# Optimization experiments

Measured on AMD Instinct MI355X. Metric: run time of the kernel, lower is better.

## Reference

```python
import jax, jax.numpy as jnp
import numpy as np

NUM_CLASSES = 20
NUM_ANCHORS = 3
BBOX_ATTRS = 5 + NUM_CLASSES
IMG_H = IMG_W = 416
IN_H = IN_W = 52
CONF_THRES = 0.5
NMS_THRES = 0.4
TOP_K = 2048


def setup_inputs() -> dict:
    key = jax.random.key(0)
    k1, _ = jax.random.split(key)
    inp = jax.random.normal(k1, (16, NUM_ANCHORS * BBOX_ATTRS, IN_H, IN_W), dtype=jnp.float32)
    anchors = jnp.array([[116.0, 90.0], [156.0, 198.0], [373.0, 326.0]], dtype=jnp.float32)
    return {"input": inp, "anchors": anchors}


def decode(inp, anchors):
    """YOLOv3 head decode (YOLOv3Loss.forward with targets=None).
    inp: [B, A*(5+C), H, W] -> output: [B, A*H*W, 5+C] with (cx, cy, w, h, conf, cls...)."""
    bs = inp.shape[0]
    stride_h = IMG_H / IN_H
    stride_w = IMG_W / IN_W
    scaled_anchors = anchors / jnp.array([stride_w, stride_h], dtype=inp.dtype)  # [A, 2]
    # [B, A, H, W, 5+C]
    pred = inp.reshape(bs, NUM_ANCHORS, BBOX_ATTRS, IN_H, IN_W).transpose(0, 1, 3, 4, 2)
    x = jax.nn.sigmoid(pred[..., 0])
    y = jax.nn.sigmoid(pred[..., 1])
    w = pred[..., 2]
    h = pred[..., 3]
    conf = jax.nn.sigmoid(pred[..., 4])
    pred_cls = jax.nn.sigmoid(pred[..., 5:])
    grid_x = jnp.arange(IN_W, dtype=inp.dtype)[None, None, None, :]
    grid_y = jnp.arange(IN_H, dtype=inp.dtype)[None, None, :, None]
    anchor_w = scaled_anchors[:, 0][None, :, None, None]
    anchor_h = scaled_anchors[:, 1][None, :, None, None]
    bx = (x + grid_x) * stride_w
    by = (y + grid_y) * stride_h
    bw = jnp.exp(w) * anchor_w * stride_w
    bh = jnp.exp(h) * anchor_h * stride_h
    boxes = jnp.stack([bx, by, bw, bh], axis=-1).reshape(bs, -1, 4)
    output = jnp.concatenate(
        [boxes, conf.reshape(bs, -1, 1), pred_cls.reshape(bs, -1, NUM_CLASSES)], axis=-1
    )
    return output


def _nms_one(corners, conf, cls_pred):
    """Greedy class-aware NMS over TOP_K conf-sorted candidates.
    corners: [K,4] x1y1x2y2, conf: [K] desc-sorted, cls_pred: [K] int32.
    Returns keep mask [K] bool."""
    x1, y1, x2, y2 = corners[:, 0], corners[:, 1], corners[:, 2], corners[:, 3]
    area = (x2 - x1 + 1.0) * (y2 - y1 + 1.0)
    ix1 = jnp.maximum(x1[:, None], x1[None, :])
    iy1 = jnp.maximum(y1[:, None], y1[None, :])
    ix2 = jnp.minimum(x2[:, None], x2[None, :])
    iy2 = jnp.minimum(y2[:, None], y2[None, :])
    inter = jnp.clip(ix2 - ix1 + 1.0, 0.0) * jnp.clip(iy2 - iy1 + 1.0, 0.0)
    iou = inter / (area[:, None] + area[None, :] - inter + 1e-16)
    # suppress j if kept i (earlier, higher conf, same class) overlaps >= thres
    cond = (iou >= NMS_THRES) & (cls_pred[:, None] == cls_pred[None, :])
    valid = conf >= CONF_THRES
    K = conf.shape[0]
    idx = jnp.arange(K)

    def body(i, carry):
        keep, supp = carry
        ki = valid[i] & (~supp[i])
        keep = keep.at[i].set(ki)
        supp = supp | (cond[i] & (idx > i) & ki)
        return keep, supp

    keep, _ = jax.lax.fori_loop(0, K, body, (jnp.zeros(K, bool), jnp.zeros(K, bool)))
    return keep


def reference(input, anchors):
    output = decode(input, anchors)  # [B, N, 5+C]
    conf = output[..., 4]
    # top-K candidates by objectness (desc order == conf sort in original NMS)
    top_conf, top_idx = jax.lax.top_k(conf, TOP_K)  # [B, K]
    boxes = output[..., :4]
    cx, cy, w, h = boxes[..., 0], boxes[..., 1], boxes[..., 2], boxes[..., 3]
    corners = jnp.stack([cx - w / 2, cy - h / 2, cx + w / 2, cy + h / 2], axis=-1)
    corners_s = jnp.take_along_axis(corners, top_idx[..., None], axis=1)  # [B, K, 4]
    cls_pred = jnp.argmax(output[..., 5:], axis=-1).astype(jnp.int32)  # [B, N]
    cls_s = jnp.take_along_axis(cls_pred, top_idx, axis=1)  # [B, K]
    keep = jax.vmap(_nms_one)(corners_s, top_conf, cls_s)  # [B, K] bool
    return output, top_idx, keep
```

## Files before the change

kernel.cpp:

```cpp
#include <hip/hip_runtime.h>

#pragma clang fp contract(off)

#define B 16
#define A 3
#define HGT 52
#define WID 52
#define HW 2704
#define NCAND 8112
#define CATTR 25
#define TOPK 2048
#define NWORD 64
#define CH 256
#define NCHUNK (TOPK / CH)
#define GPC (CH / 32)
#define CHP 260
#define EPT 8

typedef unsigned int uint32;
typedef unsigned long long u64;

__global__ __launch_bounds__(256) void decode_kernel(const float* __restrict__ inp,
                                                     const float* __restrict__ anchors,
                                                     float* __restrict__ out,
                                                     float* __restrict__ cws) {
    __shared__ float sm[256 * CATTR];
    int tid = threadIdx.x;
    int t = blockIdx.x * 256 + tid;
    int b  = t / NCAND;
    int n  = t - b * NCAND;
    int a  = n / HW;
    int hw = n - a * HW;
    int gy = hw / WID;
    int gx = hw - gy * WID;
    const float* ip = inp + ((size_t)(b * (A * CATTR) + a * CATTR)) * HW + hw;
    float* sp = sm + tid * CATTR;

    float p0 = ip[0 * HW], p1 = ip[1 * HW], p2 = ip[2 * HW], p3 = ip[3 * HW], p4 = ip[4 * HW];
    float sx = 1.0f / (1.0f + expf(-p0));
    float sy = 1.0f / (1.0f + expf(-p1));
    float bx = (sx + (float)gx) * 8.0f;
    float by = (sy + (float)gy) * 8.0f;
    float bw = expf(p2) * anchors[a * 2 + 0];
    float bh = expf(p3) * anchors[a * 2 + 1];
    float cf = 1.0f / (1.0f + expf(-p4));
    sp[0] = bx; sp[1] = by; sp[2] = bw; sp[3] = bh; sp[4] = cf;
    cws[t] = cf;
#pragma unroll
    for (int c = 0; c < 20; ++c) {
        float v = ip[(5 + c) * HW];
        sp[5 + c] = 1.0f / (1.0f + expf(-v));
    }
    __syncthreads();
    const float4* sm4 = (const float4*)sm;
    float4* o4 = (float4*)(out + (size_t)blockIdx.x * 256 * CATTR);
#pragma unroll
    for (int k = 0; k < 6; ++k) o4[k * 256 + tid] = sm4[k * 256 + tid];
    if (tid < 64) o4[1536 + tid] = sm4[1536 + tid];
}

__device__ __forceinline__ void cexd(u64& a, u64& b, bool up) {
    if ((a > b) == up) { u64 tmp = a; a = b; b = tmp; }
}

__device__ __forceinline__ u64 sel(u64 k, u64 o, bool kmin) {
    return kmin ? (k < o ? k : o) : (k > o ? k : o);
}

__device__ __forceinline__ void bitonic_merge_2048(u64 key[EPT], u64* mb, int t) {
    for (unsigned j = 1024; j >= 8; j >>= 1) {
        unsigned m = j >> 3;
        bool kmin = ((t & m) == 0);
        if (m >= 64) {
            __syncthreads();
#pragma unroll
            for (int e = 0; e < EPT; ++e) mb[e * 256 + t] = key[e];
            __syncthreads();
            int pt = t ^ (int)m;
#pragma unroll
            for (int e = 0; e < EPT; ++e) key[e] = sel(key[e], mb[e * 256 + pt], kmin);
        } else {
#pragma unroll
            for (int e = 0; e < EPT; ++e) {
                u64 o = __shfl_xor(key[e], (int)m);
                key[e] = sel(key[e], o, kmin);
            }
        }
    }
    cexd(key[0], key[4], true); cexd(key[1], key[5], true);
    cexd(key[2], key[6], true); cexd(key[3], key[7], true);
    cexd(key[0], key[2], true); cexd(key[1], key[3], true);
    cexd(key[4], key[6], true); cexd(key[5], key[7], true);
    cexd(key[0], key[1], true); cexd(key[2], key[3], true);
    cexd(key[4], key[5], true); cexd(key[6], key[7], true);
}

__global__ __launch_bounds__(256) void sort1_kernel(const float* __restrict__ conf,
                                                    u64* __restrict__ runs) {
    __shared__ u64 mb[2048];
    int blk = blockIdx.x;
    int b = blk >> 2, c = blk & 3;
    int t = threadIdx.x;
    int base = t * EPT;
    int gbase = c * 2048 + base;
    const float* cp = conf + b * NCAND;

    u64 key[EPT];
    if (gbase + EPT <= NCAND) {
        const float4* cp4 = (const float4*)(cp + gbase);
        float4 c0 = cp4[0], c1 = cp4[1];
        float cf[EPT] = {c0.x, c0.y, c0.z, c0.w, c1.x, c1.y, c1.z, c1.w};
#pragma unroll
        for (int e = 0; e < EPT; ++e) {
            unsigned bits = __float_as_uint(cf[e]) | 0x80000000u;
            key[e] = ((u64)(~bits) << 32) | (unsigned)(gbase + e);
        }
    } else {
#pragma unroll
        for (int e = 0; e < EPT; ++e) {
            int idx = gbase + e;
            if (idx < NCAND) {
                unsigned bits = __float_as_uint(cp[idx]) | 0x80000000u;
                key[e] = ((u64)(~bits) << 32) | (unsigned)idx;
            } else key[e] = ~0ull;
        }
    }

    cexd(key[0], key[1], true); cexd(key[2], key[3], false);
    cexd(key[4], key[5], true); cexd(key[6], key[7], false);

    cexd(key[0], key[2], true);  cexd(key[1], key[3], true);
    cexd(key[4], key[6], false); cexd(key[5], key[7], false);
    cexd(key[0], key[1], true);  cexd(key[2], key[3], true);
    cexd(key[4], key[5], false); cexd(key[6], key[7], false);

    bool up8 = ((t & 1) == 0);
    cexd(key[0], key[4], up8); cexd(key[1], key[5], up8);
    cexd(key[2], key[6], up8); cexd(key[3], key[7], up8);
    cexd(key[0], key[2], up8); cexd(key[1], key[3], up8);
    cexd(key[4], key[6], up8); cexd(key[5], key[7], up8);
    cexd(key[0], key[1], up8); cexd(key[2], key[3], up8);
    cexd(key[4], key[5], up8); cexd(key[6], key[7], up8);

    for (unsigned k = 16; k <= 2048; k <<= 1) {
        bool up = (((unsigned)base & k) == 0);
        for (unsigned j = k >> 1; j >= 8; j >>= 1) {
            unsigned m = j >> 3;
            bool kmin = (up == ((t & m) == 0));
            if (m >= 64) {
                __syncthreads();
#pragma unroll
                for (int e = 0; e < EPT; ++e) mb[e * 256 + t] = key[e];
                __syncthreads();
                int pt = t ^ (int)m;
#pragma unroll
                for (int e = 0; e < EPT; ++e) key[e] = sel(key[e], mb[e * 256 + pt], kmin);
            } else {
#pragma unroll
                for (int e = 0; e < EPT; ++e) {
                    u64 o = __shfl_xor(key[e], (int)m);
                    key[e] = sel(key[e], o, kmin);
                }
            }
        }
        cexd(key[0], key[4], up); cexd(key[1], key[5], up);
        cexd(key[2], key[6], up); cexd(key[3], key[7], up);
        cexd(key[0], key[2], up); cexd(key[1], key[3], up);
        cexd(key[4], key[6], up); cexd(key[5], key[7], up);
        cexd(key[0], key[1], up); cexd(key[2], key[3], up);
        cexd(key[4], key[5], up); cexd(key[6], key[7], up);
    }

    u64* R = runs + ((size_t)b * 4 + c) * 2048;
#pragma unroll
    for (int e = 0; e < EPT; ++e) R[base + e] = key[e];
}

__global__ __launch_bounds__(256) void sort23_kernel(const u64* __restrict__ runs,
                                                     const float* __restrict__ out,
                                                     float* __restrict__ topf,
                                                     float* __restrict__ gx1,
                                                     float* __restrict__ gy1,
                                                     float* __restrict__ gx2,
                                                     float* __restrict__ gy2,
                                                     float* __restrict__ gar,
                                                     uint32* __restrict__ gcv,
                                                     uint32* __restrict__ vwords) {
    __shared__ u64 mb[2048];
    __shared__ uint32 vb[256];
    int b = blockIdx.x;
    int t = threadIdx.x;
    int base = t * EPT;
    const u64* R0 = runs + (size_t)b * 4 * 2048;

    u64 ka[EPT], kb[EPT];
#pragma unroll
    for (int e = 0; e < EPT; ++e) {
        u64 a = R0[base + e];
        u64 o = R0[2048 + 2047 - (base + e)];
        ka[e] = a < o ? a : o;
    }
    bitonic_merge_2048(ka, mb, t);
#pragma unroll
    for (int e = 0; e < EPT; ++e) {
        u64 a = R0[2 * 2048 + base + e];
        u64 o = R0[3 * 2048 + 2047 - (base + e)];
        kb[e] = a < o ? a : o;
    }
    bitonic_merge_2048(kb, mb, t);
    __syncthreads();
#pragma unroll
    for (int e = 0; e < EPT; ++e) mb[base + e] = kb[e];
    __syncthreads();
#pragma unroll
    for (int e = 0; e < EPT; ++e) {
        u64 o = mb[2047 - (base + e)];
        ka[e] = ka[e] < o ? ka[e] : o;
    }
    bitonic_merge_2048(ka, mb, t);

    const float* ob = out + (size_t)b * NCAND * CATTR;
    uint32 vbits = 0;
#pragma unroll
    for (int e = 0; e < EPT; ++e) {
        uint32 idx = (uint32)(ka[e] & 0xFFFFFFFFu);
        int tg = b * TOPK + base + e;
        topf[tg] = (float)idx;
        const float* p = ob + (size_t)idx * CATTR;
        float cx = p[0], cy = p[1], w = p[2], h = p[3], cf = p[4];
        float hw_ = w * 0.5f, hh_ = h * 0.5f;
        float x1 = cx - hw_, y1 = cy - hh_, x2 = cx + hw_, y2 = cy + hh_;
        gx1[tg] = x1; gy1[tg] = y1; gx2[tg] = x2; gy2[tg] = y2;
        gar[tg] = ((x2 - x1) + 1.0f) * ((y2 - y1) + 1.0f);
        float best = p[5]; int bc = 0;
#pragma unroll
        for (int c = 1; c < 20; ++c) {
            float v = p[5 + c];
            if (v > best) { best = v; bc = c; }
        }
        gcv[tg] = (uint32)bc;
        vbits |= (cf >= 0.5f ? 1u : 0u) << e;
    }
    vb[t] = vbits;
    __syncthreads();
    if (t < 64) {
        uint32 w4 = vb[t * 4] | (vb[t * 4 + 1] << 8) | (vb[t * 4 + 2] << 16) | (vb[t * 4 + 3] << 24);
        vwords[b * 64 + t] = w4;
    }
}

#define KMID (13421772.5 / 33554432.0)
__global__ __launch_bounds__(1024) void build_kernel(const float* __restrict__ gx1,
                                                     const float* __restrict__ gy1,
                                                     const float* __restrict__ gx2,
                                                     const float* __restrict__ gy2,
                                                     const float* __restrict__ gar,
                                                     const uint32* __restrict__ gcv,
                                                     uint32* __restrict__ rowmask) {
    __shared__ float  x1s[TOPK], y1s[TOPK], x2s[TOPK], y2s[TOPK];
    __shared__ uint32 clss[TOPK];
    int bt   = blockIdx.y;
    int pr   = blockIdx.x;
    int tid  = threadIdx.x;
    int lane = tid & 63;
    int wv   = tid >> 6;
    int base = bt * TOPK;
    u64* rm64 = (u64*)(rowmask + (size_t)base * NWORD);

    for (int j = tid; j < TOPK; j += 1024) {
        int g = base + j;
        x1s[j] = gx1[g]; y1s[j] = gy1[g]; x2s[j] = gx2[g]; y2s[j] = gy2[g];
        clss[j] = gcv[g] & 0xffu;
    }
    __syncthreads();

    int r  = (wv >> 3) ? (31 - pr) : pr;
    int i0 = r * 64 + (wv & 7) * 8;

    float rx1[8], ry1[8], rx2[8], ry2[8], rar[8];
    uint32 rcl[8];
#pragma unroll
    for (int k = 0; k < 8; ++k) {
        rx1[k] = x1s[i0 + k]; ry1[k] = y1s[i0 + k];
        rx2[k] = x2s[i0 + k]; ry2[k] = y2s[i0 + k];
        rar[k] = ((rx2[k] - rx1[k]) + 1.0f) * ((ry2[k] - ry1[k]) + 1.0f);
        rcl[k] = clss[i0 + k];
    }

    int j0 = r * 64 + lane;
    float cx1 = x1s[j0], cy1 = y1s[j0], cx2 = x2s[j0], cy2 = y2s[j0];
    uint32 cc = clss[j0];

    for (int cg = r; cg < 32; ++cg) {
        float nx1 = 0.f, ny1 = 0.f, nx2 = 0.f, ny2 = 0.f; uint32 nc = 0;
        if (cg + 1 < 32) {
            int nj = (cg + 1) * 64 + lane;
            nx1 = x1s[nj]; ny1 = y1s[nj]; nx2 = x2s[nj]; ny2 = y2s[nj];
            nc = clss[nj];
        }
        float car = ((cx2 - cx1) + 1.0f) * ((cy2 - cy1) + 1.0f);
        u64 bal[8];
#pragma unroll
        for (int k = 0; k < 8; ++k) {
            float ix1 = fmaxf(rx1[k], cx1);
            float iy1 = fmaxf(ry1[k], cy1);
            float ix2 = fminf(rx2[k], cx2);
            float iy2 = fminf(ry2[k], cy2);
            float iw = fmaxf((ix2 - ix1) + 1.0f, 0.0f);
            float ih = fmaxf((iy2 - iy1) + 1.0f, 0.0f);
            float inter = iw * ih;
            float denom = ((rar[k] + car) - inter) + 1e-16f;
            bool cond = ((double)inter > KMID * (double)denom) && (cc == rcl[k]);
            bal[k] = __ballot(cond);
        }
        u64 v = bal[0];
#pragma unroll
        for (int k = 1; k < 8; ++k) if (lane == k) v = bal[k];
        if (lane < 8) rm64[(size_t)(i0 + lane) * 32 + cg] = v;
        cx1 = nx1; cy1 = ny1; cx2 = nx2; cy2 = ny2; cc = nc;
    }
}

__device__ __forceinline__ void copy_chunk(const uint32* __restrict__ rm,
                                           uint32* __restrict__ dst,
                                           int cc, int ctid) {
    const uint32* src = rm + (size_t)cc * CH * NWORD;
    int q4min = cc >> 1;
    for (int o = ctid; o < 1024; o += 960) {
        int q4 = o & 3, r = o >> 2;
        if (q4 < q4min) continue;
        const uint4* s4 = (const uint4*)(src + (size_t)r * NWORD + q4 * 16);
        uint4 v0 = s4[0], v1 = s4[1], v2 = s4[2], v3 = s4[3];
        int gi = cc * CH + r;
        int sg = gi >> 5;
        uint32 smsk = ~((2u << (gi & 31)) - 1u);
        uint32 wv[16] = {v0.x, v0.y, v0.z, v0.w, v1.x, v1.y, v1.z, v1.w,
                         v2.x, v2.y, v2.z, v2.w, v3.x, v3.y, v3.z, v3.w};
        int wbase = q4 * 16;
        uint32* dp = dst + r;
#pragma unroll
        for (int j = 0; j < 16; ++j) {
            uint32 x = wv[j];
            if (wbase + j == sg) x &= smsk;
            dp[(wbase + j) * CHP] = x;
        }
    }
}

__global__ __launch_bounds__(1024) void scan_kernel(const uint32* __restrict__ rowmask,
                                                    const uint32* __restrict__ vwords,
                                                    float* __restrict__ keepf) {
    __shared__ uint32 buf[2][64 * CHP];
    int bt  = blockIdx.x;
    int tid = threadIdx.x;
    int wv  = tid >> 6;
    int l   = tid & 63;
    const uint32* rm = rowmask + (size_t)bt * TOPK * NWORD;

    uint32 supp = 0, keepw = 0;
    if (wv == 0) supp = ~vwords[bt * 64 + l];

    if (wv > 0) copy_chunk(rm, buf[0], 0, tid - 64);
    __syncthreads();

    for (int c = 0; c < NCHUNK; ++c) {
        if (wv > 0) {
            if (c + 1 < NCHUNK) copy_chunk(rm, buf[(c + 1) & 1], c + 1, tid - 64);
        } else {
            const uint32* bp = buf[c & 1];
            uint4 sq[8];
            {
                int g0 = c * GPC;
                const uint4* sp = (const uint4*)(bp + g0 * CHP);
#pragma unroll
                for (int q = 0; q < 8; ++q) sq[q] = sp[q];
            }
            for (int gl = 0; gl < GPC; ++gl) {
                int g = c * GPC + gl;
                uint4 rwq[8];
                const uint4* rp = (const uint4*)(bp + l * CHP + gl * 32);
#pragma unroll
                for (int q = 0; q < 8; ++q) rwq[q] = rp[q];
                uint32 cur = __builtin_amdgcn_readlane(supp, g);
#pragma unroll
                for (int q = 0; q < 8; ++q) {
                    uint32 s0 = sq[q].x, s1 = sq[q].y, s2 = sq[q].z, s3 = sq[q].w;
                    int k = q * 4;
                    cur |= s0 & ((((cur >> (k + 0)) & 1u)) - 1u);
                    cur |= s1 & ((((cur >> (k + 1)) & 1u)) - 1u);
                    cur |= s2 & ((((cur >> (k + 2)) & 1u)) - 1u);
                    cur |= s3 & ((((cur >> (k + 3)) & 1u)) - 1u);
                }
                uint32 keep = ~cur;
                if (l == g) keepw = keep;
                if (gl + 1 < GPC) {
                    const uint4* sp = (const uint4*)(bp + (g + 1) * CHP + (gl + 1) * 32);
#pragma unroll
                    for (int q = 0; q < 8; ++q) sq[q] = sp[q];
                }
                uint32 upd = 0;
#pragma unroll
                for (int q = 0; q < 8; ++q) {
                    int k = q * 4;
                    upd |= rwq[q].x & (uint32)(((int)(keep << (31 - (k + 0)))) >> 31);
                    upd |= rwq[q].y & (uint32)(((int)(keep << (31 - (k + 1)))) >> 31);
                    upd |= rwq[q].z & (uint32)(((int)(keep << (31 - (k + 2)))) >> 31);
                    upd |= rwq[q].w & (uint32)(((int)(keep << (31 - (k + 3)))) >> 31);
                }
                supp |= upd;
            }
        }
        __syncthreads();
    }

    if (wv == 0) {
#pragma unroll
        for (int k = 0; k < 32; ++k)
            keepf[bt * TOPK + l * 32 + k] = (float)((keepw >> k) & 1u);
    }
}

extern "C" void kernel_launch(void* const* d_in, const int* in_sizes, int n_in,
                              void* d_out, int out_size, void* d_ws, size_t ws_size,
                              hipStream_t stream) {
    const float* inp     = (const float*)d_in[0];
    const float* anchors = (const float*)d_in[1];
    float* out   = (float*)d_out;
    float* topf  = out  + (size_t)B * NCAND * CATTR;
    float* keepf = topf + (size_t)B * TOPK;

    float*  cws = (float*)d_ws;
    float*  gx1 = cws + B * NCAND;
    float*  gy1 = gx1 + B * TOPK;
    float*  gx2 = gy1 + B * TOPK;
    float*  gy2 = gx2 + B * TOPK;
    float*  gar = gy2 + B * TOPK;
    uint32* gcv = (uint32*)(gar + B * TOPK);
    uint32* rowmask = gcv + B * TOPK;
    uint32* vwords  = rowmask + (size_t)B * TOPK * NWORD;
    u64* runs = (u64*)rowmask;

    decode_kernel<<<(B * NCAND) / 256, 256, 0, stream>>>(inp, anchors, out, cws);
    sort1_kernel<<<B * 4, 256, 0, stream>>>(cws, runs);
    sort23_kernel<<<B, 256, 0, stream>>>(runs, out, topf, gx1, gy1, gx2, gy2, gar, gcv, vwords);
    build_kernel<<<dim3(16, B), 1024, 0, stream>>>(gx1, gy1, gx2, gy2, gar, gcv, rowmask);
    scan_kernel<<<B, 1024, 0, stream>>>(rowmask, vwords, keepf);
}
```

Baseline: 186.5 us.

## Store suppression mask transposed and stream chunks via global_load_lds

The build kernel now writes the IoU suppression bitmask in a word-major (transposed) layout and applies the self/lower-triangle mask at write time. In return, the scan kernel's producer waves copy each chunk straight from global memory into LDS with the direct global_load_lds instruction, replacing the register-staged transpose and masking loop. This is meant to cut VGPR traffic and LDS write instructions in the copy path that overlaps the serial scan. The cost is narrower 32-bit scattered stores in the build kernel, and correctness depends on the LDS offset semantics of the direct-load builtin.

```diff
diff --git a/kernel.cpp b/kernel.cpp
--- a/kernel.cpp
+++ b/kernel.cpp
@@ -265,7 +265,7 @@
     int lane = tid & 63;
     int wv   = tid >> 6;
     int base = bt * TOPK;
-    u64* rm64 = (u64*)(rowmask + (size_t)base * NWORD);
+    uint32* rmT = rowmask + (size_t)base * NWORD;
 
     for (int j = tid; j < TOPK; j += 1024) {
         int g = base + j;
@@ -315,35 +315,25 @@
         }
         u64 v = bal[0];
 #pragma unroll
-        for (int k = 1; k < 8; ++k) if (lane == k) v = bal[k];
-        if (lane < 8) rm64[(size_t)(i0 + lane) * 32 + cg] = v;
+        for (int k = 1; k < 8; ++k) if ((lane & 7) == k) v = bal[k];
+        uint32 w32 = (lane & 8) ? (uint32)(v >> 32) : (uint32)v;
+        int gi = i0 + (lane & 7);
+        int wd = 2 * cg + ((lane >> 3) & 1);
+        if (wd == (gi >> 5)) w32 &= ~((2u << (gi & 31)) - 1u);
+        if (lane < 16) rmT[(size_t)wd * TOPK + gi] = w32;
         cx1 = nx1; cy1 = ny1; cx2 = nx2; cy2 = ny2; cc = nc;
     }
 }
 
-__device__ __forceinline__ void copy_chunk(const uint32* __restrict__ rm,
-                                           uint32* __restrict__ dst,
-                                           int cc, int ctid) {
-    const uint32* src = rm + (size_t)cc * CH * NWORD;
-    int q4min = cc >> 1;
-    for (int o = ctid; o < 1024; o += 960) {
-        int q4 = o & 3, r = o >> 2;
-        if (q4 < q4min) continue;
-        const uint4* s4 = (const uint4*)(src + (size_t)r * NWORD + q4 * 16);
-        uint4 v0 = s4[0], v1 = s4[1], v2 = s4[2], v3 = s4[3];
-        int gi = cc * CH + r;
-        int sg = gi >> 5;
-        uint32 smsk = ~((2u << (gi & 31)) - 1u);
-        uint32 wv[16] = {v0.x, v0.y, v0.z, v0.w, v1.x, v1.y, v1.z, v1.w,
-                         v2.x, v2.y, v2.z, v2.w, v3.x, v3.y, v3.z, v3.w};
-        int wbase = q4 * 16;
-        uint32* dp = dst + r;
-#pragma unroll
-        for (int j = 0; j < 16; ++j) {
-            uint32 x = wv[j];
-            if (wbase + j == sg) x &= smsk;
-            dp[(wbase + j) * CHP] = x;
-        }
+__device__ __forceinline__ void copy_chunk_dma(const uint32* __restrict__ rmT,
+                                               uint32* dstL, int c, int wvm1, int lane) {
+    int wmin = 8 * c;
+    for (int w = wmin + wvm1; w < 64; w += 15) {
+        const uint32* gp = rmT + (size_t)w * TOPK + c * CH + lane * 4;
+        uint32* lp = dstL + w * CHP;
+        __builtin_amdgcn_global_load_lds((const __attribute__((address_space(1))) void*)gp,
+                                         (__attribute__((address_space(3))) void*)lp,
+                                         16, 0, 0);
     }
 }
 
@@ -355,17 +345,17 @@
     int tid = threadIdx.x;
     int wv  = tid >> 6;
     int l   = tid & 63;
-    const uint32* rm = rowmask + (size_t)bt * TOPK * NWORD;
+    const uint32* rmT = rowmask + (size_t)bt * TOPK * NWORD;
 
     uint32 supp = 0, keepw = 0;
     if (wv == 0) supp = ~vwords[bt * 64 + l];
 
-    if (wv > 0) copy_chunk(rm, buf[0], 0, tid - 64);
+    if (wv > 0) copy_chunk_dma(rmT, buf[0], 0, wv - 1, l);
     __syncthreads();
 
     for (int c = 0; c < NCHUNK; ++c) {
         if (wv > 0) {
-            if (c + 1 < NCHUNK) copy_chunk(rm, buf[(c + 1) & 1], c + 1, tid - 64);
+            if (c + 1 < NCHUNK) copy_chunk_dma(rmT, buf[(c + 1) & 1], c + 1, wv - 1, l);
         } else {
             const uint32* bp = buf[c & 1];
             uint4 sq[8];
```

Measured after the change: 184.3 us. No clear change (-1.2%).
